# Kernel tuning notes

Hardware: AMD Instinct MI355X
Metric: run time of the kernel (lower is better)

The kernel has to match this reference:

```python
import jax, jax.numpy as jnp
import numpy as np
from math import floor, log2

DEPTH = 4
DIM = 1024
HEADS = 16
DIM_HEAD = 64
FF_MULT = 4
NUM_TOKENS = 32000
SEQ = 2048
MASK_VALUE = -1e10
EPS = 1e-5
ATTN_INNER = DIM_HEAD * HEADS            # 1024
FF_INNER = DIM * FF_MULT                 # 4096
FUSED = (ATTN_INNER, DIM_HEAD, DIM_HEAD, FF_INNER, FF_INNER)  # q, k, v, ff, ff_gate


def get_alibi_slopes(heads):
    def pow2_slopes(n):
        start = 2 ** (-2 ** (-(log2(n) - 3)))
        return [start * start ** i for i in range(n)]
    if log2(heads).is_integer():
        return pow2_slopes(heads)
    c = 2 ** floor(log2(heads))
    return pow2_slopes(c) + pow2_slopes(2 * c)[0::2][: heads - c]


def make_attn_bias(seq_len, heads, mask_value):
    # ALiBi variant used by this module: bias depends only on key position j
    slopes = np.array(get_alibi_slopes(heads), dtype=np.float32)[:, None, None]  # [h,1,1]
    bias = slopes * np.arange(seq_len, dtype=np.float32)[None, None, :]          # [h,1,j]
    bias = np.broadcast_to(bias, (heads, seq_len, seq_len))
    causal = np.tril(np.ones((seq_len, seq_len), dtype=bool))
    return jnp.asarray(np.where(causal, bias, mask_value), dtype=jnp.float32)


def rmsnorm(x, gamma):
    ssq = jnp.sum(jnp.square(x), axis=-1, keepdims=True)
    return jax.lax.rsqrt(ssq + EPS) * x * gamma * (x.shape[-1] ** 0.5)


def block(x, attn_bias, wi, attn_wo, ff_wo, gamma):
    h = rmsnorm(x, gamma)
    splits = np.cumsum(FUSED[:-1])
    q, k, v, ff, ff_gate = jnp.split(h @ wi, splits, axis=-1)
    b, n, _ = q.shape
    # multi-query attention: k, v have a single shared head of size DIM_HEAD
    q = q.reshape(b, n, HEADS, DIM_HEAD).transpose(0, 2, 1, 3) * (DIM_HEAD ** -0.5)
    sim = jnp.einsum('bhid,bjd->bhij', q, k) + attn_bias
    attn = jax.nn.softmax(sim, axis=-1)
    out = jnp.einsum('bhij,bjd->bhid', attn, v)
    out = out.transpose(0, 2, 1, 3).reshape(b, n, ATTN_INNER)
    attn_out = out @ attn_wo
    ff_out = (ff * jax.nn.swish(ff_gate)) @ ff_wo
    return attn_out + ff_out


def setup_inputs() -> dict:
    key = jax.random.key(0)
    ks = jax.random.split(key, 6)
    return {
        'tokens': jax.random.randint(ks[0], (1, SEQ), 0, NUM_TOKENS),
        'embedding': jax.random.normal(ks[1], (NUM_TOKENS, DIM), jnp.float32) * 0.02,
        'wi': jax.random.normal(ks[2], (DEPTH, DIM, sum(FUSED)), jnp.float32),
        'attn_wo': jax.random.normal(ks[3], (DEPTH, ATTN_INNER, DIM), jnp.float32),
        'ff_wo': jax.random.normal(ks[4], (DEPTH, FF_INNER, DIM), jnp.float32),
        'gammas': jnp.ones((DEPTH, DIM), jnp.float32),
        'final_gamma': jnp.ones((DIM,), jnp.float32),
    }


def reference(tokens, embedding, wi, attn_wo, ff_wo, gammas, final_gamma):
    n = tokens.shape[-1]
    attn_bias = make_attn_bias(SEQ, HEADS, MASK_VALUE)[..., :n, :n]
    x = embedding[tokens]                     # [b, n, dim]
    for l in range(DEPTH):
        x = block(x, attn_bias, wi[l], attn_wo[l], ff_wo[l], gammas[l]) + x
    x = rmsnorm(x, final_gamma)
    return x @ embedding.T                    # tied-embedding logits [b, n, vocab]
```

## Files before the change

### kernel.cpp

```cpp
#include <hip/hip_runtime.h>
#include <stdint.h>


typedef __attribute__((ext_vector_type(8))) __bf16 bf16x8;
typedef __attribute__((ext_vector_type(4))) __bf16 bf16x4;
typedef __attribute__((ext_vector_type(8))) short s16x8;
typedef __attribute__((ext_vector_type(4))) float f32x4;

#define SEQ   2048
#define DIM   1024
#define NHEAD 16
#define DHEAD 64
#define FUSEN 9344
#define WIN   9472
#define QKW   1088
#define FFIN  4096
#define VOCAB 32000
#define AFW   5120
#define LOG2E 1.44269504f

__device__ __forceinline__ f32x4 mfma16(bf16x8 a, bf16x8 b, f32x4 c) {
  return __builtin_amdgcn_mfma_f32_16x16x32_bf16(
      __builtin_bit_cast(s16x8, a), __builtin_bit_cast(s16x8, b), c, 0, 0, 0);
}

__device__ __forceinline__ void load_lds16(const __bf16* g, __bf16* l) {
  __builtin_amdgcn_global_load_lds(
      (const __attribute__((address_space(1))) uint32_t*)g,
      (__attribute__((address_space(3))) uint32_t*)l, 16, 0, 0);
}


__global__ void cast_k(const float* __restrict__ in, __bf16* __restrict__ out, int n8) {
  int i = blockIdx.x * 256 + threadIdx.x;
  if (i >= n8) return;
  const float4* p = (const float4*)in + (size_t)i * 2;
  float4 a = p[0], b = p[1];
  bf16x8 o;
  o[0] = (__bf16)a.x; o[1] = (__bf16)a.y; o[2] = (__bf16)a.z; o[3] = (__bf16)a.w;
  o[4] = (__bf16)b.x; o[5] = (__bf16)b.y; o[6] = (__bf16)b.z; o[7] = (__bf16)b.w;
  *(bf16x8*)(out + (size_t)i * 8) = o;
}

__global__ void gather_k(const int* __restrict__ tokens, const float* __restrict__ emb,
                         float* __restrict__ x) {
  int n = blockIdx.x;
  int tok = tokens[n];
  float4 v = ((const float4*)(emb + (size_t)tok * DIM))[threadIdx.x];
  ((float4*)(x + (size_t)n * DIM))[threadIdx.x] = v;
}

__global__ __launch_bounds__(256) void transpose_cast_k(
    const float* __restrict__ in, __bf16* __restrict__ out, int R, int C, int ldo) {
  __shared__ float tile[32][33];
  int tx = threadIdx.x & 31, ty = threadIdx.x >> 5;
  int c0 = blockIdx.x * 32, r0 = blockIdx.y * 32;
  for (int i = ty; i < 32; i += 8)
    tile[i][tx] = in[(size_t)(r0 + i) * C + c0 + tx];
  __syncthreads();
  for (int i = ty; i < 32; i += 8)
    out[(size_t)(c0 + i) * ldo + r0 + tx] = (__bf16)tile[tx][i];
}

__global__ __launch_bounds__(256) void rmsnorm_k(
    const float* __restrict__ x, const float* __restrict__ gamma, __bf16* __restrict__ h) {
  int n = blockIdx.x;
  float4 v = ((const float4*)(x + (size_t)n * DIM))[threadIdx.x];
  float ssq = v.x * v.x + v.y * v.y + v.z * v.z + v.w * v.w;
  for (int m = 32; m >= 1; m >>= 1) ssq += __shfl_xor(ssq, m, 64);
  __shared__ float red[4];
  if ((threadIdx.x & 63) == 0) red[threadIdx.x >> 6] = ssq;
  __syncthreads();
  float tot = red[0] + red[1] + red[2] + red[3];
  float rs = rsqrtf(tot + 1e-5f) * 32.0f;
  float4 g = ((const float4*)gamma)[threadIdx.x];
  bf16x4 o;
  o[0] = (__bf16)(v.x * rs * g.x);
  o[1] = (__bf16)(v.y * rs * g.y);
  o[2] = (__bf16)(v.z * rs * g.z);
  o[3] = (__bf16)(v.w * rs * g.w);
  *(bf16x4*)(h + (size_t)n * DIM + threadIdx.x * 4) = o;
}

__global__ __launch_bounds__(256) void vtrans_k(const __bf16* __restrict__ hw,
                                                __bf16* __restrict__ vT) {
  __shared__ __bf16 tile[32][33];
  int tx = threadIdx.x & 31, ty = threadIdx.x >> 5;
  int j0 = blockIdx.x * 32, d0 = blockIdx.y * 32;
  for (int i = ty; i < 32; i += 8)
    tile[i][tx] = hw[(size_t)(j0 + i) * FUSEN + 1088 + d0 + tx];
  __syncthreads();
  for (int i = ty; i < 32; i += 8)
    vT[(size_t)(d0 + i) * SEQ + j0 + tx] = tile[tx][i];
}

__global__ void act_k(const __bf16* __restrict__ hw, __bf16* __restrict__ aof) {
  int n = blockIdx.y;
  int m = (blockIdx.x * 256 + threadIdx.x) * 8;
  bf16x8 f = *(const bf16x8*)(hw + (size_t)n * FUSEN + 1152 + m);
  bf16x8 g = *(const bf16x8*)(hw + (size_t)n * FUSEN + 5248 + m);
  bf16x8 o;
#pragma unroll
  for (int i = 0; i < 8; i++) {
    float ff = (float)f[i], gg = (float)g[i];
    float s = gg / (1.f + expf(-gg));
    o[i] = (__bf16)(ff * s);
  }
  *(bf16x8*)(aof + (size_t)n * AFW + 1024 + m) = o;
}

__global__ __launch_bounds__(256) void gemm_bt_k(
    const __bf16* __restrict__ A, int lda,
    const __bf16* __restrict__ Bt, int ldb,
    float* __restrict__ outf, int ldc, int K) {
  __shared__ __bf16 lA[8192];
  __shared__ __bf16 lB[8192];
  const int t = threadIdx.x;
  const int lane = t & 63, wave = t >> 6;
  const int lo4 = lane & 15, hi2 = lane >> 4;
  const int nwg = gridDim.x * gridDim.y;
  const int orig = blockIdx.y * gridDim.x + blockIdx.x;
  const int xcd = orig & 7, off = orig >> 3;
  const int qq = nwg >> 3, rr = nwg & 7;
  const int nid = (xcd < rr ? xcd * (qq + 1) : rr * (qq + 1) + (xcd - rr) * qq) + off;
  const int bm = nid % gridDim.y, bn = nid / gridDim.y;
  const int k0 = blockIdx.z * K;
  const int wr = (wave >> 1) * 64, wc = (wave & 1) * 64;

  f32x4 acc[4][4];
#pragma unroll
  for (int m = 0; m < 4; m++)
#pragma unroll
    for (int n = 0; n < 4; n++) acc[m][n] = f32x4{0.f, 0.f, 0.f, 0.f};

  const int e0 = t * 8;
  const int e1 = 2048 + t * 8;
  const __bf16* gA0 = A + (size_t)(bm * 128 + (e0 >> 5)) * lda + (e0 & 31) + k0;
  const __bf16* gA1 = A + (size_t)(bm * 128 + (e1 >> 5)) * lda + (e1 & 31) + k0;
  const __bf16* gB0 = Bt + (size_t)(bn * 128 + (e0 >> 5)) * ldb + (e0 & 31) + k0;
  const __bf16* gB1 = Bt + (size_t)(bn * 128 + (e1 >> 5)) * ldb + (e1 & 31) + k0;
  __bf16* dA0 = &lA[wave * 512];
  __bf16* dA1 = &lA[2048 + wave * 512];
  __bf16* dB0 = &lB[wave * 512];
  __bf16* dB1 = &lB[2048 + wave * 512];

  for (int kt = 0; kt < K; kt += 64) {
    load_lds16(gA0 + kt, dA0);
    load_lds16(gA1 + kt, dA1);
    load_lds16(gB0 + kt, dB0);
    load_lds16(gB1 + kt, dB1);
    load_lds16(gA0 + kt + 32, dA0 + 4096);
    load_lds16(gA1 + kt + 32, dA1 + 4096);
    load_lds16(gB0 + kt + 32, dB0 + 4096);
    load_lds16(gB1 + kt + 32, dB1 + 4096);
    __syncthreads();
#pragma unroll
    for (int half = 0; half < 2; half++) {
      const __bf16* sA = &lA[half * 4096];
      const __bf16* sB = &lB[half * 4096];
      bf16x8 af[4], bf_[4];
#pragma unroll
      for (int m = 0; m < 4; m++)
        af[m] = *(const bf16x8*)&sA[(wr + m * 16 + lo4) * 32 + hi2 * 8];
#pragma unroll
      for (int n = 0; n < 4; n++)
        bf_[n] = *(const bf16x8*)&sB[(wc + n * 16 + lo4) * 32 + hi2 * 8];
#pragma unroll
      for (int m = 0; m < 4; m++)
#pragma unroll
        for (int n = 0; n < 4; n++)
          acc[m][n] = mfma16(af[m], bf_[n], acc[m][n]);
    }
    __syncthreads();
  }

#pragma unroll
  for (int m = 0; m < 4; m++) {
    const int rowb = bm * 128 + wr + m * 16 + hi2 * 4;
#pragma unroll
    for (int n = 0; n < 4; n++) {
      const int col = bn * 128 + wc + n * 16 + lo4;
#pragma unroll
      for (int j = 0; j < 4; j++)
        unsafeAtomicAdd(&outf[(size_t)(rowb + j) * ldc + col], acc[m][n][j]);
    }
  }
}

template <int MODE>
__global__ __launch_bounds__(512, 1) void gemm256_k(
    const __bf16* __restrict__ A, const __bf16* __restrict__ Bt,
    float* __restrict__ C, int ldc,
    __bf16* __restrict__ qh, __bf16* __restrict__ ql, __bf16* __restrict__ hw,
    int K) {
  __shared__ __bf16 lds[65536];
  const int t = threadIdx.x;
  const int lane = t & 63, w = t >> 6;
  const int lo4 = lane & 15, hi2 = lane >> 4;
  const int wr = w >> 2, wc = w & 3;
  const int nwg = gridDim.x * gridDim.y;
  const int orig = blockIdx.y * gridDim.x + blockIdx.x;
  const int xcd = orig & 7, off = orig >> 3;
  const int qq = nwg >> 3, rr = nwg & 7;
  const int nid = (xcd < rr ? xcd * (qq + 1) : rr * (qq + 1) + (xcd - rr) * qq) + off;
  const int bm = nid % gridDim.y, bn = nid / gridDim.y;

  const int srow = lane >> 2;
  const int scol = ((lane & 3) * 8) ^ ((lane >> 5) << 4);
  const __bf16* gA = A + (size_t)(bm * 256 + srow) * K + scol;
  const __bf16* gB = Bt + (size_t)(bn * 256 + srow) * K + scol;
  const int cpr = (hi2 * 8) ^ ((lo4 >= 8) ? 16 : 0);

  auto STAGE = [&](int kt, int ks, int isB) {
    const __bf16* g = (isB ? gB : gA) + kt * 64 + ks * 32;
    __bf16* l = &lds[isB * 32768 + (kt & 1) * 16384 + ks * 8192 + (2 * w) * 512];
    load_lds16(g + (size_t)(2 * w) * 16 * K, l);
    load_lds16(g + (size_t)(2 * w + 1) * 16 * K, l + 512);
  };

  f32x4 acc[8][4];
#pragma unroll
  for (int m = 0; m < 8; m++)
#pragma unroll
    for (int n = 0; n < 4; n++) acc[m][n] = f32x4{0.f, 0.f, 0.f, 0.f};

  STAGE(0, 0, 0); STAGE(0, 0, 1); STAGE(0, 1, 0); STAGE(0, 1, 1);

  const int NIT = K >> 7;
  bf16x8 bfr[4];
  for (int it = 0; it < NIT; ++it) {
#pragma unroll
    for (int p = 0; p < 8; ++p) {
      const int g = p >> 2;
      const int u = p & 3;
      const int ks = u >> 1, mh = u & 1;
      const int kt = 2 * it + g;
      const bool dostage = (it < NIT - 1) || (g == 0);
      if ((u & 1) == 0) {
        if (it == NIT - 1 && g == 1 && u == 2)
          asm volatile("s_waitcnt vmcnt(0)" ::: "memory");
        else
          asm volatile("s_waitcnt vmcnt(4)" ::: "memory");
        __builtin_amdgcn_s_barrier();
      }
      const int abase = g * 16384 + ks * 8192 + lo4 * 32 + cpr;
      if ((u & 1) == 0) {
#pragma unroll
        for (int n = 0; n < 4; n++)
          bfr[n] = *(const bf16x8*)&lds[32768 + abase + (wc * 4 + n) * 512];
      }
      bf16x8 af[4];
#pragma unroll
      for (int mm = 0; mm < 4; mm++)
        af[mm] = *(const bf16x8*)&lds[abase + (wr * 8 + mh * 4 + mm) * 512];
      if (dostage) STAGE(kt + 1, ks, u & 1);
      __builtin_amdgcn_s_setprio(1);
#pragma unroll
      for (int mm = 0; mm < 4; mm++)
#pragma unroll
        for (int n = 0; n < 4; n++)
          acc[mh * 4 + mm][n] = mfma16(af[mm], bfr[n], acc[mh * 4 + mm][n]);
      __builtin_amdgcn_s_setprio(0);
    }
  }

#pragma unroll
  for (int m = 0; m < 8; m++) {
    const int rowb = bm * 256 + wr * 128 + m * 16 + hi2 * 4;
#pragma unroll
    for (int n = 0; n < 4; n++) {
      const int col = bn * 256 + wc * 64 + n * 16 + lo4;
#pragma unroll
      for (int j = 0; j < 4; j++) {
        const int row = rowb + j;
        float v = acc[m][n][j];
        if (MODE == 0) {
          __builtin_nontemporal_store(v, &C[(size_t)row * ldc + col]);
        } else {
          if (col < QKW) {
            __bf16 hi = (__bf16)v;
            qh[(size_t)row * QKW + col] = hi;
            ql[(size_t)row * QKW + col] = (__bf16)(v - (float)hi);
          } else if (col < FUSEN) {
            hw[(size_t)row * FUSEN + col] = (__bf16)v;
          }
        }
      }
    }
  }
}

__global__ __launch_bounds__(256, 4) void flash_k(
    const __bf16* __restrict__ qh, const __bf16* __restrict__ ql,
    const __bf16* __restrict__ vT, __bf16* __restrict__ aof) {
  const int t = threadIdx.x;
  const int lane = t & 63, wave = t >> 6;
  const int lo4 = lane & 15, hi2 = lane >> 4;
  const int b = blockIdx.x;
  const int h = b & 15;
  const int s = b >> 4;
  const int pr = wave >> 1, half = wave & 1;
  const int c = pr ? (127 - s) : s;
  const int qrow0 = c * 16;
  const int nt = (c >> 2) + 1;
  const int ntA = (nt + 1) >> 1;
  const int jt0 = half ? ntA : 0;
  const int jtE = half ? nt : ntA;
  const float slope2 = exp2f(-0.5f * (float)(h + 1)) * LOG2E;
  const float scale2 = 0.125f * LOG2E;

  __shared__ __bf16 lP[4][16][72];
  __shared__ float smO[2][2][16][65];
  __shared__ float sml[2][2][16][2];
  __bf16 (*lPw)[72] = lP[wave];

  bf16x8 qhf[2], qlf[2];
#pragma unroll
  for (int kk = 0; kk < 2; kk++) {
    size_t qoff = (size_t)(qrow0 + lo4) * QKW + h * 64 + kk * 32 + hi2 * 8;
    qhf[kk] = *(const bf16x8*)(qh + qoff);
    qlf[kk] = *(const bf16x8*)(ql + qoff);
  }

  float jb[4][4];
#pragma unroll
  for (int f = 0; f < 4; f++)
#pragma unroll
    for (int r = 0; r < 4; r++)
      jb[f][r] = slope2 * (float)(jt0 * 64 + f * 16 + hi2 * 4 + r);
  const float dj = slope2 * 64.0f;
  const int iq = qrow0 + lo4;

  f32x4 O[4];
#pragma unroll
  for (int f = 0; f < 4; f++) O[f] = f32x4{0.f, 0.f, 0.f, 0.f};
  float mr = -1e30f, lr = 0.f;

  for (int jt = jt0; jt < jtE; ++jt) {
    f32x4 sc[4];
#pragma unroll
    for (int f = 0; f < 4; f++) sc[f] = f32x4{0.f, 0.f, 0.f, 0.f};
    __builtin_amdgcn_s_setprio(1);
#pragma unroll
    for (int kk = 0; kk < 2; kk++) {
#pragma unroll
      for (int f = 0; f < 4; f++) {
        size_t koff = (size_t)(jt * 64 + f * 16 + lo4) * QKW + 1024 + kk * 32 + hi2 * 8;
        bf16x8 khf = *(const bf16x8*)(qh + koff);
        bf16x8 klf = *(const bf16x8*)(ql + koff);
        sc[f] = mfma16(khf, qlf[kk], sc[f]);
        sc[f] = mfma16(klf, qhf[kk], sc[f]);
        sc[f] = mfma16(khf, qhf[kk], sc[f]);
      }
    }
    __builtin_amdgcn_s_setprio(0);

    float pv[4][4];
    float tmax = -1e30f;
#pragma unroll
    for (int f = 0; f < 4; f++)
#pragma unroll
      for (int r = 0; r < 4; r++) {
        const int j = jt * 64 + f * 16 + hi2 * 4 + r;
        float v = fmaf(sc[f][r], scale2, jb[f][r]);
        if (j > iq) v = -1e30f;
        pv[f][r] = v;
        tmax = fmaxf(tmax, v);
      }
    tmax = fmaxf(tmax, __shfl_xor(tmax, 16, 64));
    tmax = fmaxf(tmax, __shfl_xor(tmax, 32, 64));
    float mn = fmaxf(mr, tmax);
    float corr = exp2f(mr - mn);
    mr = mn;
    float rs = 0.f;
#pragma unroll
    for (int f = 0; f < 4; f++)
#pragma unroll
      for (int r = 0; r < 4; r++) {
        float pe = exp2f(pv[f][r] - mn);
        __bf16 pb = (__bf16)pe;
        lPw[lo4][f * 16 + hi2 * 4 + r] = pb;
        rs += (float)pb;
      }
    rs += __shfl_xor(rs, 16, 64);
    rs += __shfl_xor(rs, 32, 64);
    lr = lr * corr + rs;
    float co[4];
#pragma unroll
    for (int r = 0; r < 4; r++)
      co[r] = __shfl(corr, (lane & 48) + hi2 * 4 + r, 64);
#pragma unroll
    for (int f = 0; f < 4; f++)
#pragma unroll
      for (int r = 0; r < 4; r++) O[f][r] *= co[r];

    __builtin_amdgcn_s_setprio(1);
#pragma unroll
    for (int kk = 0; kk < 2; kk++) {
      bf16x8 pa = *(const bf16x8*)&lPw[lo4][kk * 32 + hi2 * 8];
#pragma unroll
      for (int f = 0; f < 4; f++) {
        bf16x8 vb = *(const bf16x8*)(vT + (size_t)(f * 16 + lo4) * SEQ + jt * 64 + kk * 32 + hi2 * 8);
        O[f] = mfma16(pa, vb, O[f]);
      }
    }
    __builtin_amdgcn_s_setprio(0);

#pragma unroll
    for (int f = 0; f < 4; f++)
#pragma unroll
      for (int r = 0; r < 4; r++) jb[f][r] += dj;
  }

#pragma unroll
  for (int f = 0; f < 4; f++)
#pragma unroll
    for (int r = 0; r < 4; r++)
      smO[pr][half][hi2 * 4 + r][f * 16 + lo4] = O[f][r];
  if (hi2 == 0) {
    sml[pr][half][lo4][0] = mr;
    sml[pr][half][lo4][1] = lr;
  }
  __syncthreads();
  if (half == 0) {
#pragma unroll
    for (int r = 0; r < 4; r++) {
      const int row = hi2 * 4 + r;
      float mA = sml[pr][0][row][0], lA = sml[pr][0][row][1];
      float mB = sml[pr][1][row][0], lB = sml[pr][1][row][1];
      float mS = fmaxf(mA, mB);
      float cA = exp2f(mA - mS), cB = exp2f(mB - mS);
      float li = lA * cA + lB * cB;
#pragma unroll
      for (int f = 0; f < 4; f++) {
        float v = (smO[pr][0][row][f * 16 + lo4] * cA +
                   smO[pr][1][row][f * 16 + lo4] * cB) / li;
        aof[(size_t)(qrow0 + row) * AFW + h * 64 + f * 16 + lo4] = (__bf16)v;
      }
    }
  }
}


extern "C" void kernel_launch(void* const* d_in, const int* in_sizes, int n_in,
                              void* d_out, int out_size, void* d_ws, size_t ws_size,
                              hipStream_t stream) {
  const int* tokens  = (const int*)d_in[0];
  const float* emb   = (const float*)d_in[1];
  const float* wi    = (const float*)d_in[2];
  const float* awo   = (const float*)d_in[3];
  const float* fwo   = (const float*)d_in[4];
  const float* gam   = (const float*)d_in[5];
  const float* fgam  = (const float*)d_in[6];
  float* out = (float*)d_out;

  char* wsp = (char*)d_ws;
  size_t woff = 0;
  auto walloc = [&](size_t b) { void* p = wsp + woff; woff += (b + 255) & ~(size_t)255; return p; };
  __bf16* embb = (__bf16*)walloc((size_t)VOCAB * DIM * 2);
  __bf16* wiT  = (__bf16*)walloc((size_t)WIN * DIM * 2);
  __bf16* BT2  = (__bf16*)walloc((size_t)DIM * AFW * 2);
  __bf16* h    = (__bf16*)walloc((size_t)SEQ * DIM * 2);

  char* op = (char*)d_out;
  size_t ooff = 0;
  auto oalloc = [&](size_t b) { void* p = op + ooff; ooff += (b + 255) & ~(size_t)255; return p; };
  float*  x     = (float*)oalloc((size_t)SEQ * DIM * 4);
  float*  y     = (float*)oalloc((size_t)SEQ * DIM * 4);
  __bf16* hw    = (__bf16*)oalloc((size_t)SEQ * FUSEN * 2);
  __bf16* qhb   = (__bf16*)oalloc((size_t)SEQ * QKW * 2);
  __bf16* qlb   = (__bf16*)oalloc((size_t)SEQ * QKW * 2);
  __bf16* vT    = (__bf16*)oalloc((size_t)DHEAD * SEQ * 2);
  __bf16* aof   = (__bf16*)oalloc((size_t)SEQ * AFW * 2);
  (void)ws_size; (void)in_sizes; (void)n_in; (void)out_size;

  cast_k<<<(VOCAB * DIM / 8 + 255) / 256, 256, 0, stream>>>(emb, embb, VOCAB * DIM / 8);
  gather_k<<<SEQ, 256, 0, stream>>>(tokens, emb, x);

  for (int l = 0; l < 4; l++) {
    transpose_cast_k<<<dim3(FUSEN / 32, DIM / 32), 256, 0, stream>>>(
        wi + (size_t)l * DIM * FUSEN, wiT, DIM, FUSEN, DIM);
    transpose_cast_k<<<dim3(DIM / 32, DIM / 32), 256, 0, stream>>>(
        awo + (size_t)l * DIM * DIM, BT2, DIM, DIM, AFW);
    transpose_cast_k<<<dim3(DIM / 32, FFIN / 32), 256, 0, stream>>>(
        fwo + (size_t)l * FFIN * DIM, BT2 + 1024, FFIN, DIM, AFW);

    rmsnorm_k<<<SEQ, 256, 0, stream>>>(x, gam + l * DIM, h);
    gemm256_k<1><<<dim3(WIN / 256, SEQ / 256), 512, 0, stream>>>(
        h, wiT, nullptr, 0, qhb, qlb, hw, DIM);
    vtrans_k<<<dim3(SEQ / 32, DHEAD / 32), 256, 0, stream>>>(hw, vT);
    flash_k<<<dim3(1024), 256, 0, stream>>>(qhb, qlb, vT, aof);
    act_k<<<dim3(FFIN / 2048, SEQ), 256, 0, stream>>>(hw, aof);
    hipMemcpyAsync(y, x, (size_t)SEQ * DIM * 4, hipMemcpyDeviceToDevice, stream);
    gemm_bt_k<<<dim3(DIM / 128, SEQ / 128, 4), 256, 0, stream>>>(
        aof, AFW, BT2, AFW, y, DIM, AFW / 4);
    float* tmp = x; x = y; y = tmp;
  }

  rmsnorm_k<<<SEQ, 256, 0, stream>>>(x, fgam, h);
  gemm256_k<0><<<dim3(VOCAB / 256, SEQ / 256), 512, 0, stream>>>(
      h, embb, out, VOCAB, nullptr, nullptr, nullptr, DIM);
}
```

Measured before the change: 1.301 ms.

## Replace atomic split-K with partial buffers fused into next RMSNorm; 128-tile fused GEMM

The output-projection GEMM now writes two split-K partials with plain stores instead of atomically accumulating into a copy of the residual. The residual add and partial reduction move into the next RMSNorm kernel, which removes the device memcpy and the atomics. The QKV/FF input GEMM switches from the 256-tile kernel padded to 9472 columns to the 128-tile kernel over exactly 9344 columns. This trades extra partial-buffer traffic, and likely less efficient small tiles on the large GEMM, for lower padding waste and no atomic contention.

Result: faster. 1.270 ms (-2.4%).

```diff
diff --git a/kernel.cpp b/kernel.cpp
--- a/kernel.cpp
+++ b/kernel.cpp
@@ -12,7 +12,6 @@
 #define NHEAD 16
 #define DHEAD 64
 #define FUSEN 9344
-#define WIN   9472
 #define QKW   1088
 #define FFIN  4096
 #define VOCAB 32000
@@ -62,10 +61,19 @@
     out[(size_t)(c0 + i) * ldo + r0 + tx] = (__bf16)tile[tx][i];
 }
 
-__global__ __launch_bounds__(256) void rmsnorm_k(
-    const float* __restrict__ x, const float* __restrict__ gamma, __bf16* __restrict__ h) {
+template <int HASP>
+__global__ __launch_bounds__(256) void rmsnorm_fuse_k(
+    const float* __restrict__ x, const float* __restrict__ p,
+    const float* __restrict__ gamma, float* __restrict__ xn,
+    __bf16* __restrict__ h) {
   int n = blockIdx.x;
   float4 v = ((const float4*)(x + (size_t)n * DIM))[threadIdx.x];
+  if (HASP) {
+    float4 a = ((const float4*)(p + (size_t)n * DIM))[threadIdx.x];
+    float4 b = ((const float4*)(p + (size_t)(SEQ + n) * DIM))[threadIdx.x];
+    v.x += a.x + b.x; v.y += a.y + b.y; v.z += a.z + b.z; v.w += a.w + b.w;
+    ((float4*)(xn + (size_t)n * DIM))[threadIdx.x] = v;
+  }
   float ssq = v.x * v.x + v.y * v.y + v.z * v.z + v.w * v.w;
   for (int m = 32; m >= 1; m >>= 1) ssq += __shfl_xor(ssq, m, 64);
   __shared__ float red[4];
@@ -109,10 +117,13 @@
   *(bf16x8*)(aof + (size_t)n * AFW + 1024 + m) = o;
 }
 
+template <int MODE>
 __global__ __launch_bounds__(256) void gemm_bt_k(
     const __bf16* __restrict__ A, int lda,
     const __bf16* __restrict__ Bt, int ldb,
-    float* __restrict__ outf, int ldc, int K) {
+    float* __restrict__ outf, int ldc,
+    __bf16* __restrict__ qh, __bf16* __restrict__ ql, __bf16* __restrict__ hw,
+    int K) {
   __shared__ __bf16 lA[8192];
   __shared__ __bf16 lB[8192];
   const int t = threadIdx.x;
@@ -174,6 +185,7 @@
     __syncthreads();
   }
 
+  float* op = outf + (size_t)blockIdx.z * SEQ * DIM;
 #pragma unroll
   for (int m = 0; m < 4; m++) {
     const int rowb = bm * 128 + wr + m * 16 + hi2 * 4;
@@ -181,18 +193,28 @@
     for (int n = 0; n < 4; n++) {
       const int col = bn * 128 + wc + n * 16 + lo4;
 #pragma unroll
-      for (int j = 0; j < 4; j++)
-        unsafeAtomicAdd(&outf[(size_t)(rowb + j) * ldc + col], acc[m][n][j]);
-    }
-  }
-}
-
-template <int MODE>
+      for (int j = 0; j < 4; j++) {
+        const int row = rowb + j;
+        float v = acc[m][n][j];
+        if (MODE == 0) {
+          __builtin_nontemporal_store(v, &op[(size_t)row * ldc + col]);
+        } else {
+          if (col < QKW) {
+            __bf16 hi = (__bf16)v;
+            qh[(size_t)row * QKW + col] = hi;
+            ql[(size_t)row * QKW + col] = (__bf16)(v - (float)hi);
+          } else {
+            hw[(size_t)row * FUSEN + col] = (__bf16)v;
+          }
+        }
+      }
+    }
+  }
+}
+
 __global__ __launch_bounds__(512, 1) void gemm256_k(
     const __bf16* __restrict__ A, const __bf16* __restrict__ Bt,
-    float* __restrict__ C, int ldc,
-    __bf16* __restrict__ qh, __bf16* __restrict__ ql, __bf16* __restrict__ hw,
-    int K) {
+    float* __restrict__ C, int ldc, int K) {
   __shared__ __bf16 lds[65536];
   const int t = threadIdx.x;
   const int lane = t & 63, w = t >> 6;
@@ -271,21 +293,8 @@
     for (int n = 0; n < 4; n++) {
       const int col = bn * 256 + wc * 64 + n * 16 + lo4;
 #pragma unroll
-      for (int j = 0; j < 4; j++) {
-        const int row = rowb + j;
-        float v = acc[m][n][j];
-        if (MODE == 0) {
-          __builtin_nontemporal_store(v, &C[(size_t)row * ldc + col]);
-        } else {
-          if (col < QKW) {
-            __bf16 hi = (__bf16)v;
-            qh[(size_t)row * QKW + col] = hi;
-            ql[(size_t)row * QKW + col] = (__bf16)(v - (float)hi);
-          } else if (col < FUSEN) {
-            hw[(size_t)row * FUSEN + col] = (__bf16)v;
-          }
-        }
-      }
+      for (int j = 0; j < 4; j++)
+        __builtin_nontemporal_store(acc[m][n][j], &C[(size_t)(rowb + j) * ldc + col]);
     }
   }
 }
@@ -458,15 +467,16 @@
   size_t woff = 0;
   auto walloc = [&](size_t b) { void* p = wsp + woff; woff += (b + 255) & ~(size_t)255; return p; };
   __bf16* embb = (__bf16*)walloc((size_t)VOCAB * DIM * 2);
-  __bf16* wiT  = (__bf16*)walloc((size_t)WIN * DIM * 2);
+  __bf16* wiT  = (__bf16*)walloc((size_t)FUSEN * DIM * 2);
   __bf16* BT2  = (__bf16*)walloc((size_t)DIM * AFW * 2);
   __bf16* h    = (__bf16*)walloc((size_t)SEQ * DIM * 2);
 
   char* op = (char*)d_out;
   size_t ooff = 0;
   auto oalloc = [&](size_t b) { void* p = op + ooff; ooff += (b + 255) & ~(size_t)255; return p; };
-  float*  x     = (float*)oalloc((size_t)SEQ * DIM * 4);
-  float*  y     = (float*)oalloc((size_t)SEQ * DIM * 4);
+  float*  xA    = (float*)oalloc((size_t)SEQ * DIM * 4);
+  float*  xB    = (float*)oalloc((size_t)SEQ * DIM * 4);
+  float*  pp    = (float*)oalloc((size_t)2 * SEQ * DIM * 4);
   __bf16* hw    = (__bf16*)oalloc((size_t)SEQ * FUSEN * 2);
   __bf16* qhb   = (__bf16*)oalloc((size_t)SEQ * QKW * 2);
   __bf16* qlb   = (__bf16*)oalloc((size_t)SEQ * QKW * 2);
@@ -475,8 +485,10 @@
   (void)ws_size; (void)in_sizes; (void)n_in; (void)out_size;
 
   cast_k<<<(VOCAB * DIM / 8 + 255) / 256, 256, 0, stream>>>(emb, embb, VOCAB * DIM / 8);
-  gather_k<<<SEQ, 256, 0, stream>>>(tokens, emb, x);
-
+  gather_k<<<SEQ, 256, 0, stream>>>(tokens, emb, xA);
+
+  float* x = xA;
+  float* xn = xB;
   for (int l = 0; l < 4; l++) {
     transpose_cast_k<<<dim3(FUSEN / 32, DIM / 32), 256, 0, stream>>>(
         wi + (size_t)l * DIM * FUSEN, wiT, DIM, FUSEN, DIM);
@@ -485,19 +497,22 @@
     transpose_cast_k<<<dim3(DIM / 32, FFIN / 32), 256, 0, stream>>>(
         fwo + (size_t)l * FFIN * DIM, BT2 + 1024, FFIN, DIM, AFW);
 
-    rmsnorm_k<<<SEQ, 256, 0, stream>>>(x, gam + l * DIM, h);
-    gemm256_k<1><<<dim3(WIN / 256, SEQ / 256), 512, 0, stream>>>(
-        h, wiT, nullptr, 0, qhb, qlb, hw, DIM);
+    if (l == 0) {
+      rmsnorm_fuse_k<0><<<SEQ, 256, 0, stream>>>(x, nullptr, gam, nullptr, h);
+    } else {
+      rmsnorm_fuse_k<1><<<SEQ, 256, 0, stream>>>(x, pp, gam + l * DIM, xn, h);
+      float* tmp = x; x = xn; xn = tmp;
+    }
+    gemm_bt_k<1><<<dim3(FUSEN / 128, SEQ / 128), 256, 0, stream>>>(
+        h, DIM, wiT, DIM, nullptr, 0, qhb, qlb, hw, DIM);
     vtrans_k<<<dim3(SEQ / 32, DHEAD / 32), 256, 0, stream>>>(hw, vT);
     flash_k<<<dim3(1024), 256, 0, stream>>>(qhb, qlb, vT, aof);
     act_k<<<dim3(FFIN / 2048, SEQ), 256, 0, stream>>>(hw, aof);
-    hipMemcpyAsync(y, x, (size_t)SEQ * DIM * 4, hipMemcpyDeviceToDevice, stream);
-    gemm_bt_k<<<dim3(DIM / 128, SEQ / 128, 4), 256, 0, stream>>>(
-        aof, AFW, BT2, AFW, y, DIM, AFW / 4);
-    float* tmp = x; x = y; y = tmp;
-  }
-
-  rmsnorm_k<<<SEQ, 256, 0, stream>>>(x, fgam, h);
-  gemm256_k<0><<<dim3(VOCAB / 256, SEQ / 256), 512, 0, stream>>>(
-      h, embb, out, VOCAB, nullptr, nullptr, nullptr, DIM);
-}
+    gemm_bt_k<0><<<dim3(DIM / 128, SEQ / 128, 2), 256, 0, stream>>>(
+        aof, AFW, BT2, AFW, pp, DIM, nullptr, nullptr, nullptr, AFW / 2);
+  }
+
+  rmsnorm_fuse_k<1><<<SEQ, 256, 0, stream>>>(x, pp, fgam, xn, h);
+  gemm256_k<<<dim3(VOCAB / 256, SEQ / 256), 512, 0, stream>>>(
+      h, embb, out, VOCAB, DIM);
+}
```
